# Kernel optimization log

Measured on AMD Instinct MI355X. Metric: run time of the kernel, lower is better.

Reference implementation:

```python
import jax, jax.numpy as jnp
import numpy as np

DIM_LATENT = 256
NUM_ATOM_TYPES = 16
NUM_EDGE_TYPES = 4
HIDDEN = 256
HIDDEN_FINAL = 256
BS, N = 8, 256


def setup_inputs() -> dict:
    key = jax.random.key(0)
    ks = jax.random.split(key, 12)
    s = lambda fan_in: 1.0 / np.sqrt(fan_in)
    return {
        "latent": jax.random.normal(ks[0], (BS, N, DIM_LATENT), jnp.float32),
        "positions": jax.random.normal(ks[1], (BS, N, 3), jnp.float32),
        "atom_types": jax.random.uniform(ks[2], (BS, N, NUM_ATOM_TYPES), jnp.float32),
        # latent_mlp: Linear(dim_latent, hidden) -> ReLU -> Linear(hidden, hidden)
        "W1": jax.random.uniform(ks[3], (DIM_LATENT, HIDDEN), jnp.float32, -s(DIM_LATENT), s(DIM_LATENT)),
        "b1": jax.random.uniform(ks[4], (HIDDEN,), jnp.float32, -s(DIM_LATENT), s(DIM_LATENT)),
        "W2": jax.random.uniform(ks[5], (HIDDEN, HIDDEN), jnp.float32, -s(HIDDEN), s(HIDDEN)),
        "b2": jax.random.uniform(ks[6], (HIDDEN,), jnp.float32, -s(HIDDEN), s(HIDDEN)),
        # final_mlp: Linear(1+num_atom_types+dim_latent, hidden_final) -> ReLU -> Linear(hidden_final, num_edge_types)
        "W3": jax.random.uniform(ks[7], (1 + NUM_ATOM_TYPES + DIM_LATENT, HIDDEN_FINAL), jnp.float32, -s(1 + NUM_ATOM_TYPES + DIM_LATENT), s(1 + NUM_ATOM_TYPES + DIM_LATENT)),
        "b3": jax.random.uniform(ks[8], (HIDDEN_FINAL,), jnp.float32, -s(1 + NUM_ATOM_TYPES + DIM_LATENT), s(1 + NUM_ATOM_TYPES + DIM_LATENT)),
        "W4": jax.random.uniform(ks[9], (HIDDEN_FINAL, NUM_EDGE_TYPES), jnp.float32, -s(HIDDEN_FINAL), s(HIDDEN_FINAL)),
        "b4": jax.random.uniform(ks[10], (NUM_EDGE_TYPES,), jnp.float32, -s(HIDDEN_FINAL), s(HIDDEN_FINAL)),
    }


def _pairwise_dist(positions):
    # torch.cdist (euclidean), grad-safe sqrt (zero on the diagonal)
    diff = positions[:, :, None, :] - positions[:, None, :, :]  # bs x n x n x 3
    d2 = jnp.sum(diff * diff, axis=-1)
    safe = jnp.where(d2 > 0, d2, 1.0)
    return jnp.where(d2 > 0, jnp.sqrt(safe), 0.0)


def reference(latent, positions, atom_types, W1, b1, W2, b2, W3, b3, W4, b4):
    # latent_mlp
    h = jax.nn.relu(latent @ W1 + b1) @ W2 + b2  # bs x n x hidden (== dim_latent)
    dist = _pairwise_dist(positions)[..., None]  # bs x n x n x 1
    atom_pairs = atom_types[:, :, None, :] * atom_types[:, None, :, :]  # bs x n x n x A
    latent_pairs = h[:, :, None, :] * h[:, None, :, :]                  # bs x n x n x C
    y = jnp.concatenate((dist, atom_pairs, latent_pairs), axis=3)
    return jax.nn.relu(y @ W3 + b3) @ W4 + b4  # bs x n x n x num_edge_types
```

## Files before the change

### kernel.cpp

```cpp
#include <hip/hip_runtime.h>

#define DIM 256
#define NA 16
#define NE 4
#define KTOT 288

typedef __attribute__((ext_vector_type(8))) short short8;
typedef __attribute__((ext_vector_type(4))) float f32x4;

static __device__ __forceinline__ ushort f2bf(float f) {
  union { float f; unsigned int u; } v; v.f = f;
  unsigned int r = (v.u + 0x7FFFu + ((v.u >> 16) & 1u)) >> 16;
  return (ushort)r;
}

static __device__ __forceinline__ float bf2f(ushort s) {
  union { unsigned int u; float f; } v; v.u = ((unsigned int)s) << 16;
  return v.f;
}

static __device__ __forceinline__ unsigned cvtpk(float lo, float hi) {
  unsigned r;
  asm("v_cvt_pk_bf16_f32 %0, %1, %2" : "=v"(r) : "v"(lo), "v"(hi));
  return r;
}

static __device__ __forceinline__ int fragIdx(int row, int c) {
  return (((row >> 4)*9 + (c >> 5))*4 + ((c >> 3) & 3))*128 + (row & 15)*8 + (c & 7);
}

__global__ __launch_bounds__(256) void prep_h_kernel(
    const float* __restrict__ latent, const float* __restrict__ atoms,
    const float* __restrict__ W1, const float* __restrict__ b1,
    const float* __restrict__ W2, const float* __restrict__ b2,
    ushort* __restrict__ Gf) {
  __shared__ float lat[8][DIM];
  __shared__ float t1[8][DIM];
  const int b = blockIdx.x >> 5, i0 = (blockIdx.x & 31) * 8;
  const int k = threadIdx.x;
  #pragma unroll
  for (int r = 0; r < 8; ++r) lat[r][k] = latent[(b*256 + i0 + r) * DIM + k];
  __syncthreads();
  float acc[8];
  #pragma unroll
  for (int r = 0; r < 8; ++r) acc[r] = b1[k];
  for (int c = 0; c < DIM; c += 4) {
    float w0 = W1[(c+0)*DIM + k], w1 = W1[(c+1)*DIM + k];
    float w2 = W1[(c+2)*DIM + k], w3 = W1[(c+3)*DIM + k];
    #pragma unroll
    for (int r = 0; r < 8; ++r) {
      const float4 l4 = *reinterpret_cast<const float4*>(&lat[r][c]);
      acc[r] += l4.x*w0 + l4.y*w1 + l4.z*w2 + l4.w*w3;
    }
  }
  #pragma unroll
  for (int r = 0; r < 8; ++r) t1[r][k] = fmaxf(acc[r], 0.f);
  __syncthreads();
  #pragma unroll
  for (int r = 0; r < 8; ++r) acc[r] = b2[k];
  for (int c = 0; c < DIM; c += 4) {
    float w0 = W2[(c+0)*DIM + k], w1 = W2[(c+1)*DIM + k];
    float w2 = W2[(c+2)*DIM + k], w3 = W2[(c+3)*DIM + k];
    #pragma unroll
    for (int r = 0; r < 8; ++r) {
      const float4 l4 = *reinterpret_cast<const float4*>(&t1[r][c]);
      acc[r] += l4.x*w0 + l4.y*w1 + l4.z*w2 + l4.w*w3;
    }
  }
  #pragma unroll
  for (int r = 0; r < 8; ++r) {
    int row = b*256 + i0 + r;
    Gf[fragIdx(row, NA + k)] = f2bf(acc[r]);
  }
  if (k < NA) {
    #pragma unroll
    for (int r = 0; r < 8; ++r) {
      int row = b*256 + i0 + r;
      Gf[fragIdx(row, k)] = f2bf(atoms[row*NA + k]);
      Gf[fragIdx(row, 272 + k)] = 0;
    }
  }
}

__global__ __launch_bounds__(256) void prep_w3t_kernel(
    const float* __restrict__ W3, ushort* __restrict__ W3Tf) {
  const int n = blockIdx.x, c = threadIdx.x;
  W3Tf[fragIdx(n, c)] = (c < 272) ? f2bf(W3[(1+c)*DIM + n]) : (ushort)0;
  if (c < 32) {
    int c2 = 256 + c;
    W3Tf[fragIdx(n, c2)] = (c2 < 272) ? f2bf(W3[(1+c2)*DIM + n]) : (ushort)0;
  }
}

__global__ __attribute__((amdgpu_flat_work_group_size(256,256), amdgpu_waves_per_eu(3,3)))
void edge_main_kernel(
    const float* __restrict__ positions,
    const float* __restrict__ W3, const float* __restrict__ b3,
    const float* __restrict__ W4, const float* __restrict__ b4,
    const ushort* __restrict__ Gf, const ushort* __restrict__ W3Tf,
    float* __restrict__ out) {
  __shared__ ushort gi_lds[4608];
  __shared__ ushort gj_lds[4608];
  __shared__ float partial[4][64][4];
  __shared__ float dist_lds[64];

  const int bid = blockIdx.x;
  const int b = bid / 544;
  int rem = bid - b*544;
  const int qq4 = rem & 3;
  int q = rem >> 2;
  int it = 0;
  while (q >= 16 - it) { q -= 16 - it; ++it; }
  const int jt = it + q;
  const int i0 = b*256 + it*16, j0 = b*256 + jt*16;
  const int rbi = i0 >> 4, rbj = j0 >> 4;

  const int tid = threadIdx.x;
  const int lane = tid & 63, w = tid >> 6;
  const int c15 = lane & 15, hi = lane >> 4;

  {
    const uint4* srcI = reinterpret_cast<const uint4*>(Gf + (size_t)rbi*4608);
    const uint4* srcJ = reinterpret_cast<const uint4*>(Gf + (size_t)rbj*4608);
    uint4* dI = reinterpret_cast<uint4*>(gi_lds);
    uint4* dJ = reinterpret_cast<uint4*>(gj_lds);
    dI[tid] = srcI[tid];
    dJ[tid] = srcJ[tid];
    dI[256+tid] = srcI[256+tid];
    dJ[256+tid] = srcJ[256+tid];
    if (tid < 64) { dI[512+tid] = srcI[512+tid]; dJ[512+tid] = srcJ[512+tid]; }
  }
  if (tid < 64) {
    int pi = tid >> 4, pj = tid & 15;
    const float* pa = &positions[(i0 + qq4*4 + pi)*3];
    const float* pb = &positions[(j0 + pj)*3];
    float dx = pa[0]-pb[0], dy = pa[1]-pb[1], dz = pa[2]-pb[2];
    float d2 = dx*dx + dy*dy + dz*dz;
    dist_lds[tid] = d2 > 0.f ? sqrtf(d2) : 0.f;
  }

  f32x4 acc[4][4];
  #pragma unroll
  for (int at = 0; at < 4; ++at)
    #pragma unroll
    for (int bt = 0; bt < 4; ++bt) { acc[at][bt].x=0.f; acc[at][bt].y=0.f; acc[at][bt].z=0.f; acc[at][bt].w=0.f; }

  __syncthreads();

  #pragma unroll
  for (int kk = 0; kk < 9; ++kk) {
    union { ushort us[8]; short8 s8; } gj;
    gj.s8 = *reinterpret_cast<const short8*>(&gj_lds[kk*512 + lane*8]);
    float gjf[8];
    #pragma unroll
    for (int s = 0; s < 8; ++s) gjf[s] = bf2f(gj.us[s]);
    short8 bbv[4];
    #pragma unroll
    for (int bt = 0; bt < 4; ++bt) {
      union { ushort us[8]; short8 s8; } gi;
      gi.s8 = *reinterpret_cast<const short8*>(
          &gi_lds[kk*512 + hi*128 + (qq4*4 + bt)*8]);
      union { unsigned uu[4]; short8 s8; } bb;
      bb.uu[0] = cvtpk(bf2f(gi.us[0])*gjf[0], bf2f(gi.us[1])*gjf[1]);
      bb.uu[1] = cvtpk(bf2f(gi.us[2])*gjf[2], bf2f(gi.us[3])*gjf[3]);
      bb.uu[2] = cvtpk(bf2f(gi.us[4])*gjf[4], bf2f(gi.us[5])*gjf[5]);
      bb.uu[3] = cvtpk(bf2f(gi.us[6])*gjf[6], bf2f(gi.us[7])*gjf[7]);
      bbv[bt] = bb.s8;
    }
    #pragma unroll
    for (int at = 0; at < 4; ++at) {
      short8 af = *reinterpret_cast<const short8*>(
          &W3Tf[((w*4 + at)*9 + kk)*512 + lane*8]);
      acc[at][0] = __builtin_amdgcn_mfma_f32_16x16x32_bf16(af, bbv[0], acc[at][0], 0, 0, 0);
      acc[at][1] = __builtin_amdgcn_mfma_f32_16x16x32_bf16(af, bbv[1], acc[at][1], 0, 0, 0);
      acc[at][2] = __builtin_amdgcn_mfma_f32_16x16x32_bf16(af, bbv[2], acc[at][2], 0, 0, 0);
      acc[at][3] = __builtin_amdgcn_mfma_f32_16x16x32_bf16(af, bbv[3], acc[at][3], 0, 0, 0);
    }
  }

  __builtin_amdgcn_sched_barrier(0);

  float4 pe[4];
  #pragma unroll
  for (int bt = 0; bt < 4; ++bt) { pe[bt].x=0.f; pe[bt].y=0.f; pe[bt].z=0.f; pe[bt].w=0.f; }
  #pragma unroll
  for (int at = 0; at < 4; ++at) {
    float b3v[4], w30v[4]; float4 w4v[4];
    #pragma unroll
    for (int r = 0; r < 4; ++r) {
      int n = (w*4 + at)*16 + hi*4 + r;
      b3v[r]  = b3[n];
      w30v[r] = W3[n];
      w4v[r]  = *reinterpret_cast<const float4*>(&W4[n*4]);
    }
    #pragma unroll
    for (int bt = 0; bt < 4; ++bt) {
      float d = dist_lds[bt*16 + c15];
      #pragma unroll
      for (int r = 0; r < 4; ++r) {
        float z  = acc[at][bt][r] + d*w30v[r] + b3v[r];
        float rz = fmaxf(z, 0.f);
        pe[bt].x += rz*w4v[r].x; pe[bt].y += rz*w4v[r].y;
        pe[bt].z += rz*w4v[r].z; pe[bt].w += rz*w4v[r].w;
      }
    }
  }
  #pragma unroll
  for (int bt = 0; bt < 4; ++bt) {
    int pair = bt*16 + c15;
    float4 p = pe[bt];
    p.x += __shfl_xor(p.x, 16); p.y += __shfl_xor(p.y, 16);
    p.z += __shfl_xor(p.z, 16); p.w += __shfl_xor(p.w, 16);
    p.x += __shfl_xor(p.x, 32); p.y += __shfl_xor(p.y, 32);
    p.z += __shfl_xor(p.z, 32); p.w += __shfl_xor(p.w, 32);
    if (hi == 0) *reinterpret_cast<float4*>(&partial[w][pair][0]) = p;
  }
  __syncthreads();
  if (tid < 64) {
    int pair = tid;
    float4 v;
    v.x = partial[0][pair][0] + partial[1][pair][0] + partial[2][pair][0] + partial[3][pair][0];
    v.y = partial[0][pair][1] + partial[1][pair][1] + partial[2][pair][1] + partial[3][pair][1];
    v.z = partial[0][pair][2] + partial[1][pair][2] + partial[2][pair][2] + partial[3][pair][2];
    v.w = partial[0][pair][3] + partial[1][pair][3] + partial[2][pair][3] + partial[3][pair][3];
    const float4 bv = *reinterpret_cast<const float4*>(b4);
    v.x += bv.x; v.y += bv.y; v.z += bv.z; v.w += bv.w;
    int il = it*16 + qq4*4 + (pair >> 4);
    int jl = jt*16 + (pair & 15);
    *reinterpret_cast<float4*>(&out[(((size_t)b*256 + il)*256 + jl)*NE]) = v;
    if (it != jt)
      *reinterpret_cast<float4*>(&out[(((size_t)b*256 + jl)*256 + il)*NE]) = v;
  }
}

extern "C" void kernel_launch(void* const* d_in, const int* in_sizes, int n_in,
                              void* d_out, int out_size, void* d_ws, size_t ws_size,
                              hipStream_t stream) {
  const float* latent    = (const float*)d_in[0];
  const float* positions = (const float*)d_in[1];
  const float* atoms     = (const float*)d_in[2];
  const float* W1 = (const float*)d_in[3];
  const float* b1 = (const float*)d_in[4];
  const float* W2 = (const float*)d_in[5];
  const float* b2 = (const float*)d_in[6];
  const float* W3 = (const float*)d_in[7];
  const float* b3 = (const float*)d_in[8];
  const float* W4 = (const float*)d_in[9];
  const float* b4 = (const float*)d_in[10];
  float* out = (float*)d_out;

  char* ws = (char*)d_ws;
  ushort* Gf_ws   = (ushort*)ws;
  ushort* W3Tf_ws = (ushort*)(ws + 1179648);

  hipLaunchKernelGGL(prep_h_kernel, dim3(256), dim3(256), 0, stream,
                     latent, atoms, W1, b1, W2, b2, Gf_ws);
  hipLaunchKernelGGL(prep_w3t_kernel, dim3(256), dim3(256), 0, stream, W3, W3Tf_ws);
  hipLaunchKernelGGL(edge_main_kernel, dim3(4352), dim3(256), 0, stream,
                     positions, W3, b3, W4, b4, Gf_ws, W3Tf_ws, out);
}
```

Baseline: 100.3 us.

## Precompute pair-product B fragments once into padded LDS instead of per-wave

Each block used to stage the i-row and j-row latent fragments in LDS, and all four waves then recomputed the same bf16 pairwise products for the MFMA B operands. Now each thread computes its share of the products directly from global memory once, during staging, and stores them in a padded LDS layout (stride 5 chunks) to avoid bank conflicts. The MFMA loop then only does LDS loads. This removes the 4x redundant convert/multiply work, but the staged buffer is larger (about 46KB), which may cut occupancy, and the global reads are less contiguous.

```diff
diff --git a/kernel.cpp b/kernel.cpp
--- a/kernel.cpp
+++ b/kernel.cpp
@@ -99,8 +99,7 @@
     const float* __restrict__ W4, const float* __restrict__ b4,
     const ushort* __restrict__ Gf, const ushort* __restrict__ W3Tf,
     float* __restrict__ out) {
-  __shared__ ushort gi_lds[4608];
-  __shared__ ushort gj_lds[4608];
+  __shared__ ushort y_lds[9*64*5*8];
   __shared__ float partial[4][64][4];
   __shared__ float dist_lds[64];
 
@@ -120,15 +119,23 @@
   const int c15 = lane & 15, hi = lane >> 4;
 
   {
-    const uint4* srcI = reinterpret_cast<const uint4*>(Gf + (size_t)rbi*4608);
-    const uint4* srcJ = reinterpret_cast<const uint4*>(Gf + (size_t)rbj*4608);
-    uint4* dI = reinterpret_cast<uint4*>(gi_lds);
-    uint4* dJ = reinterpret_cast<uint4*>(gj_lds);
-    dI[tid] = srcI[tid];
-    dJ[tid] = srcJ[tid];
-    dI[256+tid] = srcI[256+tid];
-    dJ[256+tid] = srcJ[256+tid];
-    if (tid < 64) { dI[512+tid] = srcI[512+tid]; dJ[512+tid] = srcJ[512+tid]; }
+    const int p = tid >> 2, oct = tid & 3;
+    const int ri = qq4*4 + (p >> 4);
+    const int rj = p & 15;
+    const ushort* giB = &Gf[(size_t)(rbi*9)*512 + oct*128 + ri*8];
+    const ushort* gjB = &Gf[(size_t)(rbj*9)*512 + oct*128 + rj*8];
+    #pragma unroll
+    for (int kk = 0; kk < 9; ++kk) {
+      union { ushort us[8]; short8 s8; } gi, gj;
+      gi.s8 = *reinterpret_cast<const short8*>(giB + kk*512);
+      gj.s8 = *reinterpret_cast<const short8*>(gjB + kk*512);
+      union { unsigned uu[4]; short8 s8; } pk;
+      pk.uu[0] = cvtpk(bf2f(gi.us[0])*bf2f(gj.us[0]), bf2f(gi.us[1])*bf2f(gj.us[1]));
+      pk.uu[1] = cvtpk(bf2f(gi.us[2])*bf2f(gj.us[2]), bf2f(gi.us[3])*bf2f(gj.us[3]));
+      pk.uu[2] = cvtpk(bf2f(gi.us[4])*bf2f(gj.us[4]), bf2f(gi.us[5])*bf2f(gj.us[5]));
+      pk.uu[3] = cvtpk(bf2f(gi.us[6])*bf2f(gj.us[6]), bf2f(gi.us[7])*bf2f(gj.us[7]));
+      *reinterpret_cast<short8*>(&y_lds[((kk*64 + p)*5 + oct)*8]) = pk.s8;
+    }
   }
   if (tid < 64) {
     int pi = tid >> 4, pj = tid & 15;
@@ -149,24 +156,11 @@
 
   #pragma unroll
   for (int kk = 0; kk < 9; ++kk) {
-    union { ushort us[8]; short8 s8; } gj;
-    gj.s8 = *reinterpret_cast<const short8*>(&gj_lds[kk*512 + lane*8]);
-    float gjf[8];
-    #pragma unroll
-    for (int s = 0; s < 8; ++s) gjf[s] = bf2f(gj.us[s]);
     short8 bbv[4];
     #pragma unroll
-    for (int bt = 0; bt < 4; ++bt) {
-      union { ushort us[8]; short8 s8; } gi;
-      gi.s8 = *reinterpret_cast<const short8*>(
-          &gi_lds[kk*512 + hi*128 + (qq4*4 + bt)*8]);
-      union { unsigned uu[4]; short8 s8; } bb;
-      bb.uu[0] = cvtpk(bf2f(gi.us[0])*gjf[0], bf2f(gi.us[1])*gjf[1]);
-      bb.uu[1] = cvtpk(bf2f(gi.us[2])*gjf[2], bf2f(gi.us[3])*gjf[3]);
-      bb.uu[2] = cvtpk(bf2f(gi.us[4])*gjf[4], bf2f(gi.us[5])*gjf[5]);
-      bb.uu[3] = cvtpk(bf2f(gi.us[6])*gjf[6], bf2f(gi.us[7])*gjf[7]);
-      bbv[bt] = bb.s8;
-    }
+    for (int bt = 0; bt < 4; ++bt)
+      bbv[bt] = *reinterpret_cast<const short8*>(
+          &y_lds[((kk*64 + bt*16 + c15)*5 + hi)*8]);
     #pragma unroll
     for (int at = 0; at < 4; ++at) {
       short8 af = *reinterpret_cast<const short8*>(
```

After: 115.6 us. 1.15x slower.
